# Kernel tuning notes

Hardware: AMD Instinct MI355X
Metric: run time of the kernel (lower is better)

Reference implementation:

```python
import jax, jax.numpy as jnp
import numpy as np

B, S, D_IN, D_OUT, H = 2, 2048, 1024, 1024, 16
DH = D_OUT // H

def setup_inputs() -> dict:
    key = jax.random.key(0)
    ks = jax.random.split(key, 6)
    sc = 0.02
    return {
        'x': jax.random.normal(ks[0], (B, S, D_IN), dtype=jnp.float32),
        'Wq': jax.random.normal(ks[1], (D_IN, D_OUT), dtype=jnp.float32) * sc,
        'Wk': jax.random.normal(ks[2], (D_IN, D_OUT), dtype=jnp.float32) * sc,
        'Wv': jax.random.normal(ks[3], (D_IN, D_OUT), dtype=jnp.float32) * sc,
        'Wo': jax.random.normal(ks[4], (D_OUT, D_OUT), dtype=jnp.float32) * sc,
        'bo': jax.random.normal(ks[5], (D_OUT,), dtype=jnp.float32) * sc,
    }

def reference(x, Wq, Wk, Wv, Wo, bo):
    b, s, _ = x.shape
    # projections, split heads: (b, h, s, dh)
    q = (x @ Wq).reshape(b, s, H, DH).transpose(0, 2, 1, 3)
    k = (x @ Wk).reshape(b, s, H, DH).transpose(0, 2, 1, 3)
    v = (x @ Wv).reshape(b, s, H, DH).transpose(0, 2, 1, 3)
    scores = jnp.einsum('bhqd,bhkd->bhqk', q, k)
    causal = jnp.triu(jnp.ones((s, s), dtype=bool), k=1)
    scores = jnp.where(causal, -jnp.inf, scores)
    attn = jax.nn.softmax(scores / jnp.sqrt(jnp.float32(DH)), axis=-1)
    ctx = jnp.einsum('bhqk,bhkd->bhqd', attn, v)
    ctx = ctx.transpose(0, 2, 1, 3).reshape(b, s, D_OUT)
    return ctx @ Wo + bo
```

## Files before the change

### kernel.cpp

```cpp
#include <hip/hip_runtime.h>
#include <hip/hip_bf16.h>
#include <cstdint>

typedef __attribute__((ext_vector_type(8))) __bf16 bf16x8;
typedef __attribute__((ext_vector_type(4))) float f32x4;
typedef __attribute__((ext_vector_type(8))) unsigned short u16x8;
typedef __attribute__((ext_vector_type(4))) unsigned short u16x4;
typedef __attribute__((ext_vector_type(4))) unsigned int u32x4;

#define NEG_INF (-__builtin_inff())

__device__ __forceinline__ unsigned short f2bf(float f) {
    unsigned int u = __builtin_bit_cast(unsigned int, f);
    u += 0x7FFFu + ((u >> 16) & 1u);
    return (unsigned short)(u >> 16);
}
__device__ __forceinline__ float bf2f(unsigned short u) {
    return __builtin_bit_cast(float, (unsigned int)u << 16);
}

__device__ __forceinline__ void gload16(const void* g, void* l) {
    __builtin_amdgcn_global_load_lds(
        (__attribute__((address_space(1))) void*)(uintptr_t)g,
        (__attribute__((address_space(3))) void*)(uint32_t)(uintptr_t)l, 16, 0, 0);
}

__global__ void cast_x_kernel(const float* __restrict__ x, unsigned short* __restrict__ xb) {
    size_t i = (size_t)blockIdx.x * 256 + threadIdx.x;
    const float4* p = (const float4*)x + i * 2;
    float4 a = p[0], c = p[1];
    u16x8 o;
    o[0] = f2bf(a.x); o[1] = f2bf(a.y); o[2] = f2bf(a.z); o[3] = f2bf(a.w);
    o[4] = f2bf(c.x); o[5] = f2bf(c.y); o[6] = f2bf(c.z); o[7] = f2bf(c.w);
    ((u16x8*)xb)[i] = o;
}

__global__ void castT_w_kernel(const float* __restrict__ W0, const float* __restrict__ W1,
                               const float* __restrict__ W2, const float* __restrict__ W3,
                               unsigned short* __restrict__ Wcat, unsigned short* __restrict__ Wot) {
    __shared__ float t[32][33];
    int z = blockIdx.z;
    const float* src = (z == 0) ? W0 : (z == 1) ? W1 : (z == 2) ? W2 : W3;
    unsigned short* dst = (z < 3) ? (Wcat + (size_t)z * 1024 * 1024) : Wot;
    int n0 = blockIdx.x * 32, k0 = blockIdx.y * 32;
    int tx = threadIdx.x & 31, ty = threadIdx.x >> 5;
    #pragma unroll
    for (int i = 0; i < 4; ++i) {
        int r = ty + i * 8;
        t[r][tx] = src[(size_t)(k0 + r) * 1024 + n0 + tx];
    }
    __syncthreads();
    #pragma unroll
    for (int i = 0; i < 4; ++i) {
        int r = ty + i * 8;
        dst[(size_t)(n0 + r) * 1024 + k0 + tx] = f2bf(t[tx][r]);
    }
}

__global__ __launch_bounds__(256, 2)
void gemm_qkv_kernel(const unsigned short* __restrict__ A, const unsigned short* __restrict__ Bt,
                     unsigned short* __restrict__ Qb, unsigned short* __restrict__ Kb,
                     unsigned short* __restrict__ Vtb) {
    __shared__ unsigned short As[128 * 64];
    __shared__ unsigned short Bs[128 * 64];
    const int tid = threadIdx.x;
    const int w = tid >> 6, l = tid & 63;
    const int lr = l & 15, lg = l >> 4;
    const int wr = w >> 1, wc = w & 1;
    const int id = blockIdx.y * 24 + blockIdx.x;
    const int swz = (id & 7) * 96 + (id >> 3);
    const int m0 = (swz / 24) * 128;
    const int n0 = (swz % 24) * 128;
    const int K = 1024;

    f32x4 acc[4][4] = {};

    for (int k0 = 0; k0 < 1024; k0 += 64) {
        #pragma unroll
        for (int p = 0; p < 4; ++p) {
            int seg = p * 4 + w;
            int row = seg * 8 + (l >> 3);
            int c16 = (l & 7) ^ (row & 7);
            gload16(A  + (size_t)(m0 + row) * K + k0 + c16 * 8, &As[seg * 512]);
            gload16(Bt + (size_t)(n0 + row) * K + k0 + c16 * 8, &Bs[seg * 512]);
        }
        __syncthreads();
        #pragma unroll
        for (int ks = 0; ks < 2; ++ks) {
            bf16x8 af[4], bfr[4];
            #pragma unroll
            for (int i = 0; i < 4; ++i) {
                int ra = wr * 64 + i * 16 + lr;
                af[i] = *(const bf16x8*)&As[ra * 64 + (((ks << 2) | lg) ^ (ra & 7)) * 8];
                int rb = wc * 64 + i * 16 + lr;
                bfr[i] = *(const bf16x8*)&Bs[rb * 64 + (((ks << 2) | lg) ^ (rb & 7)) * 8];
            }
            #pragma unroll
            for (int i = 0; i < 4; ++i)
                #pragma unroll
                for (int j = 0; j < 4; ++j)
                    acc[i][j] = __builtin_amdgcn_mfma_f32_16x16x32_bf16(af[i], bfr[j], acc[i][j], 0, 0, 0);
        }
        __syncthreads();
    }

    const int seg = n0 >> 10;
    const int n0l = n0 & 1023;
    if (seg < 2) {
        unsigned short* C = (seg == 0) ? Qb : Kb;
        const float sc = (seg == 0) ? 0.125f * 1.44269504f : 1.0f;
        #pragma unroll
        for (int i = 0; i < 4; ++i)
            #pragma unroll
            for (int j = 0; j < 4; ++j) {
                int n = n0l + wc * 64 + j * 16 + lr;
                #pragma unroll
                for (int r = 0; r < 4; ++r) {
                    int m = m0 + wr * 64 + i * 16 + lg * 4 + r;
                    C[(size_t)m * 1024 + n] = f2bf(acc[i][j][r] * sc);
                }
            }
    } else {
        #pragma unroll
        for (int i = 0; i < 4; ++i)
            #pragma unroll
            for (int j = 0; j < 4; ++j) {
                int n = n0l + wc * 64 + j * 16 + lr;
                int mb = m0 + wr * 64 + i * 16 + lg * 4;
                int bb = mb >> 11, s = mb & 2047;
                int s6 = s & 63;
                int kp = (((s6 >> 4) & 1) << 5) | (((s6 >> 2) & 3) << 3) | (((s6 >> 5) & 1) << 2);
                int sp = (s & ~63) | kp;
                u16x4 o;
                #pragma unroll
                for (int r = 0; r < 4; ++r) o[r] = f2bf(acc[i][j][r]);
                *(u16x4*)&Vtb[((size_t)(bb * 1024 + n)) * 2048 + sp] = o;
            }
    }
}

static __device__ const unsigned char QS_TAB[24] = {
    7,15,14,14,13,6,12,5,
    15,13,12,10,11,10,11,9,
    0,1,2,3,8,8,9,4};
static __device__ const unsigned char TY_TAB[24] = {
    0,2,1,2,2,0,2,0,
    1,1,1,1,1,2,2,2,
    0,0,0,0,1,2,1,0};

__global__ __launch_bounds__(256, 4)
void flash_attn_kernel(const unsigned short* __restrict__ Q, const unsigned short* __restrict__ Kg,
                       const unsigned short* __restrict__ Vt, unsigned short* __restrict__ ctx,
                       unsigned short* __restrict__ P_O, float* __restrict__ P_ml) {
    __shared__ unsigned short Ks[2][4096];
    __shared__ unsigned short Vs[2][4096];
    const int tid = threadIdx.x, w = tid >> 6, l = tid & 63;
    const int lr = l & 15, lg = l >> 4;

    const int level = blockIdx.x >> 5;
    const int bh = blockIdx.x & 31;
    const int qs = QS_TAB[level], ty = TY_TAB[level];
    const int Tf = 2 * qs + 2, mid = qs + 1;
    const int t0 = (ty == 2) ? mid : 0;
    const int t1 = (ty == 1) ? mid : Tf;
    const int b = bh >> 4, h = bh & 15;
    const int qw = qs * 128 + w * 32;

    const int srow8 = w * 8 + (l >> 3);
    const int scol  = (l & 7) ^ (srow8 & 7);
    const unsigned short* Kbase = Kg + (size_t)(b * 2048) * 1024 + h * 64;
    const unsigned short* Vbase = Vt + (size_t)(b * 1024 + h * 64) * 2048;

    const __bf16 one = (__bf16)1.0f;
    const bf16x8 ones = {one, one, one, one, one, one, one, one};

    bf16x8 qf[2][2];
    #pragma unroll
    for (int mi = 0; mi < 2; ++mi)
        #pragma unroll
        for (int ks = 0; ks < 2; ++ks)
            qf[mi][ks] = *(const bf16x8*)&Q[(size_t)(b * 2048 + qw + mi * 16 + lr) * 1024 + h * 64 + ks * 32 + lg * 8];

    float mrow[2] = {NEG_INF, NEG_INF};
    f32x4 lacc[2] = {};
    f32x4 oacc[2][4] = {};

    #pragma unroll
    for (int p = 0; p < 2; ++p)
        gload16(Kbase + (size_t)(t0 * 64 + p * 32 + srow8) * 1024 + scol * 8, &Ks[0][(p * 32 + w * 8) * 64]);

    for (int t = t0; t < t1; ++t) {
        const int cur = (t - t0) & 1;
        const int k0 = t * 64;
        #pragma unroll
        for (int p = 0; p < 2; ++p)
            gload16(Vbase + (size_t)(p * 32 + srow8) * 2048 + k0 + scol * 8, &Vs[cur][(p * 32 + w * 8) * 64]);
        const int ktn = (t + 1 < t1) ? t + 1 : t0;
        #pragma unroll
        for (int p = 0; p < 2; ++p)
            gload16(Kbase + (size_t)(ktn * 64 + p * 32 + srow8) * 1024 + scol * 8, &Ks[cur ^ 1][(p * 32 + w * 8) * 64]);

        asm volatile("s_waitcnt vmcnt(4)" ::: "memory");
        __builtin_amdgcn_s_barrier();

        f32x4 sf[2][4] = {};
        #pragma unroll
        for (int ks = 0; ks < 2; ++ks) {
            bf16x8 kf[4];
            #pragma unroll
            for (int ni = 0; ni < 4; ++ni) {
                int rk = ni * 16 + lr;
                kf[ni] = *(const bf16x8*)&Ks[cur][rk * 64 + (((ks << 2) | lg) ^ (rk & 7)) * 8];
            }
            #pragma unroll
            for (int ni = 0; ni < 4; ++ni)
                #pragma unroll
                for (int mi = 0; mi < 2; ++mi)
                    sf[mi][ni] = __builtin_amdgcn_mfma_f32_16x16x32_bf16(kf[ni], qf[mi][ks], sf[mi][ni], 0, 0, 0);
        }

        u32x4 pa0u[2], pa1u[2];
        #pragma unroll
        for (int mi = 0; mi < 2; ++mi) {
            if (t >= Tf - 2) {
                #pragma unroll
                for (int ni = 0; ni < 4; ++ni)
                    #pragma unroll
                    for (int r = 0; r < 4; ++r)
                        if (k0 + ni * 16 + lg * 4 + r > qw + mi * 16 + lr) sf[mi][ni][r] = NEG_INF;
            }
            float vmax = fmaxf(fmaxf(fmaxf(sf[mi][0][0], sf[mi][0][1]), fmaxf(sf[mi][0][2], sf[mi][0][3])),
                               fmaxf(fmaxf(sf[mi][1][0], sf[mi][1][1]), fmaxf(sf[mi][1][2], sf[mi][1][3])));
            vmax = fmaxf(vmax, fmaxf(fmaxf(fmaxf(sf[mi][2][0], sf[mi][2][1]), fmaxf(sf[mi][2][2], sf[mi][2][3])),
                                     fmaxf(fmaxf(sf[mi][3][0], sf[mi][3][1]), fmaxf(sf[mi][3][2], sf[mi][3][3]))));
            vmax = fmaxf(vmax, __shfl_xor(vmax, 16));
            vmax = fmaxf(vmax, __shfl_xor(vmax, 32));
            if (!__all(vmax <= mrow[mi] + 8.0f)) {
                float mn = fmaxf(mrow[mi], vmax);
                float av = __builtin_amdgcn_exp2f(mrow[mi] - mn);
                mrow[mi] = mn;
                float avr[4];
                #pragma unroll
                for (int r = 0; r < 4; ++r) avr[r] = __shfl(av, lg * 4 + r);
                #pragma unroll
                for (int ni = 0; ni < 4; ++ni)
                    #pragma unroll
                    for (int r = 0; r < 4; ++r)
                        oacc[mi][ni][r] *= avr[r];
                #pragma unroll
                for (int r = 0; r < 4; ++r) lacc[mi][r] *= avr[r];
            }
            #pragma unroll
            for (int ni = 0; ni < 4; ++ni)
                #pragma unroll
                for (int r = 0; r < 4; ++r)
                    sf[mi][ni][r] = __builtin_amdgcn_exp2f(sf[mi][ni][r] - mrow[mi]);

            asm("v_cvt_pk_bf16_f32 %0, %1, %2" : "=v"(pa0u[mi][0]) : "v"(sf[mi][0][0]), "v"(sf[mi][0][1]));
            asm("v_cvt_pk_bf16_f32 %0, %1, %2" : "=v"(pa0u[mi][1]) : "v"(sf[mi][0][2]), "v"(sf[mi][0][3]));
            asm("v_cvt_pk_bf16_f32 %0, %1, %2" : "=v"(pa0u[mi][2]) : "v"(sf[mi][2][0]), "v"(sf[mi][2][1]));
            asm("v_cvt_pk_bf16_f32 %0, %1, %2" : "=v"(pa0u[mi][3]) : "v"(sf[mi][2][2]), "v"(sf[mi][2][3]));
            asm("v_cvt_pk_bf16_f32 %0, %1, %2" : "=v"(pa1u[mi][0]) : "v"(sf[mi][1][0]), "v"(sf[mi][1][1]));
            asm("v_cvt_pk_bf16_f32 %0, %1, %2" : "=v"(pa1u[mi][1]) : "v"(sf[mi][1][2]), "v"(sf[mi][1][3]));
            asm("v_cvt_pk_bf16_f32 %0, %1, %2" : "=v"(pa1u[mi][2]) : "v"(sf[mi][3][0]), "v"(sf[mi][3][1]));
            asm("v_cvt_pk_bf16_f32 %0, %1, %2" : "=v"(pa1u[mi][3]) : "v"(sf[mi][3][2]), "v"(sf[mi][3][3]));

            lacc[mi] = __builtin_amdgcn_mfma_f32_16x16x32_bf16(
                __builtin_bit_cast(bf16x8, pa0u[mi]), ones, lacc[mi], 0, 0, 0);
            lacc[mi] = __builtin_amdgcn_mfma_f32_16x16x32_bf16(
                __builtin_bit_cast(bf16x8, pa1u[mi]), ones, lacc[mi], 0, 0, 0);
        }

        asm volatile("s_waitcnt vmcnt(2)" ::: "memory");
        __builtin_amdgcn_s_barrier();

        #pragma unroll
        for (int ks = 0; ks < 2; ++ks) {
            bf16x8 vb[4];
            #pragma unroll
            for (int ni = 0; ni < 4; ++ni) {
                int rv = ni * 16 + lr;
                vb[ni] = *(const bf16x8*)&Vs[cur][rv * 64 + (((ks << 2) | lg) ^ (rv & 7)) * 8];
            }
            #pragma unroll
            for (int mi = 0; mi < 2; ++mi) {
                bf16x8 pa = __builtin_bit_cast(bf16x8, ks ? pa1u[mi] : pa0u[mi]);
                #pragma unroll
                for (int ni = 0; ni < 4; ++ni)
                    oacc[mi][ni] = __builtin_amdgcn_mfma_f32_16x16x32_bf16(pa, vb[ni], oacc[mi][ni], 0, 0, 0);
            }
        }
    }

    if (ty == 0) {
        #pragma unroll
        for (int mi = 0; mi < 2; ++mi)
            #pragma unroll
            for (int r = 0; r < 4; ++r) {
                float inv = 1.0f / lacc[mi][r];
                int q = qw + mi * 16 + lg * 4 + r;
                size_t base = (size_t)(b * 2048 + q) * 1024 + h * 64 + lr;
                #pragma unroll
                for (int ni = 0; ni < 4; ++ni)
                    ctx[base + ni * 16] = f2bf(oacc[mi][ni][r] * inv);
            }
    } else {
        const int pidx = ((qs - 8) * 32 + bh) * 2 + (ty - 1);
        unsigned short* po = P_O + (size_t)pidx * 8192;
        #pragma unroll
        for (int mi = 0; mi < 2; ++mi)
            #pragma unroll
            for (int r = 0; r < 4; ++r) {
                int rowl = w * 32 + mi * 16 + lg * 4 + r;
                #pragma unroll
                for (int ni = 0; ni < 4; ++ni)
                    po[rowl * 64 + ni * 16 + lr] = f2bf(oacc[mi][ni][r]);
            }
        if (lg == 0) {
            #pragma unroll
            for (int mi = 0; mi < 2; ++mi)
                P_ml[pidx * 256 + (w * 32 + mi * 16 + lr) * 2] = mrow[mi];
        }
        if (lr == 0) {
            #pragma unroll
            for (int mi = 0; mi < 2; ++mi)
                #pragma unroll
                for (int r = 0; r < 4; ++r)
                    P_ml[pidx * 256 + (w * 32 + mi * 16 + lg * 4 + r) * 2 + 1] = lacc[mi][r];
        }
    }
}

__global__ __launch_bounds__(256)
void combine_kernel(const unsigned short* __restrict__ P_O, const float* __restrict__ P_ml,
                    unsigned short* __restrict__ ctx) {
    const int qs = 8 + (blockIdx.x >> 5);
    const int bh = blockIdx.x & 31;
    const int b = bh >> 4, h = bh & 15;
    const int p0 = ((qs - 8) * 32 + bh) * 2, p1 = p0 + 1;
    const int t = threadIdx.x;
    const int row = t >> 1, half = t & 1;
    const float m0 = P_ml[p0 * 256 + row * 2], l0 = P_ml[p0 * 256 + row * 2 + 1];
    const float m1 = P_ml[p1 * 256 + row * 2], l1 = P_ml[p1 * 256 + row * 2 + 1];
    const float m = fmaxf(m0, m1);
    float f0 = __builtin_amdgcn_exp2f(m0 - m);
    float f1 = __builtin_amdgcn_exp2f(m1 - m);
    const float inv = 1.0f / (l0 * f0 + l1 * f1);
    f0 *= inv; f1 *= inv;
    const u16x8* o0 = (const u16x8*)&P_O[(size_t)p0 * 8192 + row * 64 + half * 32];
    const u16x8* o1 = (const u16x8*)&P_O[(size_t)p1 * 8192 + row * 64 + half * 32];
    unsigned short* dst = ctx + (size_t)(b * 2048 + qs * 128 + row) * 1024 + h * 64 + half * 32;
    #pragma unroll
    for (int v = 0; v < 4; ++v) {
        u16x8 a = o0[v], c = o1[v], o;
        #pragma unroll
        for (int j = 0; j < 8; ++j)
            o[j] = f2bf(bf2f(a[j]) * f0 + bf2f(c[j]) * f1);
        ((u16x8*)dst)[v] = o;
    }
}

__global__ __launch_bounds__(256, 2)
void gemm_out_kernel(const unsigned short* __restrict__ A, const unsigned short* __restrict__ Bt,
                     float* __restrict__ C, const float* __restrict__ bias) {
    __shared__ unsigned short As[128 * 64];
    __shared__ unsigned short Bs[128 * 64];
    const int tid = threadIdx.x;
    const int w = tid >> 6, l = tid & 63;
    const int lr = l & 15, lg = l >> 4;
    const int wr = w >> 1, wc = w & 1;
    const int id = blockIdx.y * 8 + blockIdx.x;
    const int swz = (id & 7) * 32 + (id >> 3);
    const int m0 = (swz / 8) * 128;
    const int n0 = (swz % 8) * 128;
    const int K = 1024;

    f32x4 acc[4][4] = {};

    for (int k0 = 0; k0 < 1024; k0 += 64) {
        #pragma unroll
        for (int p = 0; p < 4; ++p) {
            int seg = p * 4 + w;
            int row = seg * 8 + (l >> 3);
            int c16 = (l & 7) ^ (row & 7);
            gload16(A  + (size_t)(m0 + row) * K + k0 + c16 * 8, &As[seg * 512]);
            gload16(Bt + (size_t)(n0 + row) * K + k0 + c16 * 8, &Bs[seg * 512]);
        }
        __syncthreads();
        #pragma unroll
        for (int ks = 0; ks < 2; ++ks) {
            bf16x8 af[4], bfr[4];
            #pragma unroll
            for (int i = 0; i < 4; ++i) {
                int ra = wr * 64 + i * 16 + lr;
                af[i] = *(const bf16x8*)&As[ra * 64 + (((ks << 2) | lg) ^ (ra & 7)) * 8];
                int rb = wc * 64 + i * 16 + lr;
                bfr[i] = *(const bf16x8*)&Bs[rb * 64 + (((ks << 2) | lg) ^ (rb & 7)) * 8];
            }
            #pragma unroll
            for (int i = 0; i < 4; ++i)
                #pragma unroll
                for (int j = 0; j < 4; ++j)
                    acc[i][j] = __builtin_amdgcn_mfma_f32_16x16x32_bf16(af[i], bfr[j], acc[i][j], 0, 0, 0);
        }
        __syncthreads();
    }

    #pragma unroll
    for (int i = 0; i < 4; ++i)
        #pragma unroll
        for (int j = 0; j < 4; ++j) {
            int n = n0 + wc * 64 + j * 16 + lr;
            float bv = bias[n];
            #pragma unroll
            for (int r = 0; r < 4; ++r) {
                int m = m0 + wr * 64 + i * 16 + lg * 4 + r;
                C[(size_t)m * 1024 + n] = acc[i][j][r] + bv;
            }
        }
}

extern "C" void kernel_launch(void* const* d_in, const int* in_sizes, int n_in,
                              void* d_out, int out_size, void* d_ws, size_t ws_size,
                              hipStream_t stream) {
    (void)in_sizes; (void)n_in; (void)out_size; (void)ws_size;
    const float* x  = (const float*)d_in[0];
    const float* Wq = (const float*)d_in[1];
    const float* Wk = (const float*)d_in[2];
    const float* Wv = (const float*)d_in[3];
    const float* Wo = (const float*)d_in[4];
    const float* bo = (const float*)d_in[5];
    float* out = (float*)d_out;

    char* ws = (char*)d_ws;
    const size_t MB = 1024 * 1024;
    unsigned short* xb   = (unsigned short*)(ws);
    unsigned short* Wcat = (unsigned short*)(ws + 8  * MB);
    unsigned short* Wot  = (unsigned short*)(ws + 14 * MB);
    unsigned short* Qb   = (unsigned short*)(ws + 16 * MB);
    unsigned short* Kb   = (unsigned short*)(ws + 24 * MB);
    unsigned short* Vtb  = (unsigned short*)(ws + 32 * MB);
    unsigned short* Cxb  = (unsigned short*)(ws + 40 * MB);

    unsigned short* P_O  = (unsigned short*)(ws);
    float*          P_ml = (float*)(ws + 8 * MB);

    cast_x_kernel<<<2048, 256, 0, stream>>>(x, xb);
    castT_w_kernel<<<dim3(32, 32, 4), 256, 0, stream>>>(Wq, Wk, Wv, Wo, Wcat, Wot);
    gemm_qkv_kernel<<<dim3(24, 32), 256, 0, stream>>>(xb, Wcat, Qb, Kb, Vtb);
    flash_attn_kernel<<<768, 256, 0, stream>>>(Qb, Kb, Vtb, Cxb, P_O, P_ml);
    combine_kernel<<<256, 256, 0, stream>>>(P_O, P_ml, Cxb);
    gemm_out_kernel<<<dim3(8, 32), 256, 0, stream>>>(Cxb, Wot, out, bo);
}
```

Measured before the change: 97.84 us.

## Split long causal query tiles into up to three KV chunks with three-way combine

Replaces the 2-way split-KV scheme (applied only to query tiles 8-15) with a finer one: tiles 5-10 split into two KV chunks and tiles 11-15 into three, giving 1024 attention blocks that are more evenly balanced. Chunk 0 writes unnormalized output straight into ctx and the other chunks go to a partial buffer, so the combine kernel reads ctx in place and merges two or three partials using the saved max and sum statistics. The aim is to shorten the tail of the causal workload and fill the GPU better. The cost is more partial traffic, a larger combine launch and extra bf16 rounding of the intermediate outputs.

```diff
diff --git a/kernel.cpp b/kernel.cpp
--- a/kernel.cpp
+++ b/kernel.cpp
@@ -139,14 +139,16 @@
     }
 }
 
-static __device__ const unsigned char QS_TAB[24] = {
-    7,15,14,14,13,6,12,5,
-    15,13,12,10,11,10,11,9,
-    0,1,2,3,8,8,9,4};
-static __device__ const unsigned char TY_TAB[24] = {
-    0,2,1,2,2,0,2,0,
-    1,1,1,1,1,2,2,2,
-    0,0,0,0,1,2,1,0};
+static __device__ const unsigned char QS_TAB[32] = {
+    15,15,14,14,14,15,13,13,
+    10,10,13, 9, 9,12,12, 8,
+     4,12,11,11,11, 7, 8, 7,
+     0, 1, 5, 5, 2, 6, 6, 3};
+static __device__ const unsigned char CI_TAB[32] = {
+     1, 2, 0, 1, 2, 0, 0, 1,
+     0, 1, 2, 0, 1, 1, 2, 0,
+     0, 0, 0, 1, 2, 0, 1, 1,
+     0, 0, 0, 1, 0, 0, 1, 0};
 
 __global__ __launch_bounds__(256, 4)
 void flash_attn_kernel(const unsigned short* __restrict__ Q, const unsigned short* __restrict__ Kg,
@@ -159,10 +161,11 @@
 
     const int level = blockIdx.x >> 5;
     const int bh = blockIdx.x & 31;
-    const int qs = QS_TAB[level], ty = TY_TAB[level];
-    const int Tf = 2 * qs + 2, mid = qs + 1;
-    const int t0 = (ty == 2) ? mid : 0;
-    const int t1 = (ty == 1) ? mid : Tf;
+    const int qs = QS_TAB[level], ci = CI_TAB[level];
+    const int c  = (qs >= 11) ? 3 : (qs >= 5 ? 2 : 1);
+    const int Tf = 2 * qs + 2;
+    const int t0 = (Tf * ci) / c;
+    const int t1 = (Tf * (ci + 1)) / c;
     const int b = bh >> 4, h = bh & 15;
     const int qw = qs * 128 + w * 32;
 
@@ -292,7 +295,7 @@
         }
     }
 
-    if (ty == 0) {
+    if (c == 1) {
         #pragma unroll
         for (int mi = 0; mi < 2; ++mi)
             #pragma unroll
@@ -305,28 +308,43 @@
                     ctx[base + ni * 16] = f2bf(oacc[mi][ni][r] * inv);
             }
     } else {
-        const int pidx = ((qs - 8) * 32 + bh) * 2 + (ty - 1);
-        unsigned short* po = P_O + (size_t)pidx * 8192;
-        #pragma unroll
-        for (int mi = 0; mi < 2; ++mi)
-            #pragma unroll
-            for (int r = 0; r < 4; ++r) {
-                int rowl = w * 32 + mi * 16 + lg * 4 + r;
-                #pragma unroll
-                for (int ni = 0; ni < 4; ++ni)
-                    po[rowl * 64 + ni * 16 + lr] = f2bf(oacc[mi][ni][r]);
-            }
+        if (ci == 0) {
+            #pragma unroll
+            for (int mi = 0; mi < 2; ++mi)
+                #pragma unroll
+                for (int r = 0; r < 4; ++r) {
+                    int q = qw + mi * 16 + lg * 4 + r;
+                    size_t base = (size_t)(b * 2048 + q) * 1024 + h * 64 + lr;
+                    #pragma unroll
+                    for (int ni = 0; ni < 4; ++ni)
+                        ctx[base + ni * 16] = f2bf(oacc[mi][ni][r]);
+                }
+        } else {
+            const int poslot = (qs <= 10) ? (qs - 5) : (6 + (qs - 11) * 2 + (ci - 1));
+            unsigned short* po = P_O + (size_t)(bh * 16 + poslot) * 8192;
+            #pragma unroll
+            for (int mi = 0; mi < 2; ++mi)
+                #pragma unroll
+                for (int r = 0; r < 4; ++r) {
+                    int rowl = w * 32 + mi * 16 + lg * 4 + r;
+                    #pragma unroll
+                    for (int ni = 0; ni < 4; ++ni)
+                        po[rowl * 64 + ni * 16 + lr] = f2bf(oacc[mi][ni][r]);
+                }
+        }
+        const int mlbase = (qs <= 10) ? (qs - 5) * 2 : (12 + (qs - 11) * 3);
+        float* mlp = P_ml + (size_t)(bh * 27 + mlbase + ci) * 256;
         if (lg == 0) {
             #pragma unroll
             for (int mi = 0; mi < 2; ++mi)
-                P_ml[pidx * 256 + (w * 32 + mi * 16 + lr) * 2] = mrow[mi];
+                mlp[(w * 32 + mi * 16 + lr) * 2] = mrow[mi];
         }
         if (lr == 0) {
             #pragma unroll
             for (int mi = 0; mi < 2; ++mi)
                 #pragma unroll
                 for (int r = 0; r < 4; ++r)
-                    P_ml[pidx * 256 + (w * 32 + mi * 16 + lg * 4 + r) * 2 + 1] = lacc[mi][r];
+                    mlp[(w * 32 + mi * 16 + lg * 4 + r) * 2 + 1] = lacc[mi][r];
         }
     }
 }
@@ -334,28 +352,48 @@
 __global__ __launch_bounds__(256)
 void combine_kernel(const unsigned short* __restrict__ P_O, const float* __restrict__ P_ml,
                     unsigned short* __restrict__ ctx) {
-    const int qs = 8 + (blockIdx.x >> 5);
+    const int qs = 5 + (blockIdx.x >> 5);
     const int bh = blockIdx.x & 31;
     const int b = bh >> 4, h = bh & 15;
-    const int p0 = ((qs - 8) * 32 + bh) * 2, p1 = p0 + 1;
+    const int c = (qs >= 11) ? 3 : 2;
     const int t = threadIdx.x;
     const int row = t >> 1, half = t & 1;
-    const float m0 = P_ml[p0 * 256 + row * 2], l0 = P_ml[p0 * 256 + row * 2 + 1];
-    const float m1 = P_ml[p1 * 256 + row * 2], l1 = P_ml[p1 * 256 + row * 2 + 1];
-    const float m = fmaxf(m0, m1);
-    float f0 = __builtin_amdgcn_exp2f(m0 - m);
-    float f1 = __builtin_amdgcn_exp2f(m1 - m);
-    const float inv = 1.0f / (l0 * f0 + l1 * f1);
-    f0 *= inv; f1 *= inv;
-    const u16x8* o0 = (const u16x8*)&P_O[(size_t)p0 * 8192 + row * 64 + half * 32];
-    const u16x8* o1 = (const u16x8*)&P_O[(size_t)p1 * 8192 + row * 64 + half * 32];
+
+    const int mlbase = (qs <= 10) ? (qs - 5) * 2 : (12 + (qs - 11) * 3);
+    float mv[3], lv[3];
+    #pragma unroll
+    for (int ci = 0; ci < 3; ++ci) {
+        if (ci < c) {
+            const float* mlp = P_ml + (size_t)(bh * 27 + mlbase + ci) * 256 + row * 2;
+            mv[ci] = mlp[0]; lv[ci] = mlp[1];
+        } else { mv[ci] = NEG_INF; lv[ci] = 0.0f; }
+    }
+    float m = fmaxf(fmaxf(mv[0], mv[1]), mv[2]);
+    float f0 = __builtin_amdgcn_exp2f(mv[0] - m);
+    float f1 = __builtin_amdgcn_exp2f(mv[1] - m);
+    float f2 = (c == 3) ? __builtin_amdgcn_exp2f(mv[2] - m) : 0.0f;
+    const float inv = 1.0f / (lv[0] * f0 + lv[1] * f1 + lv[2] * f2);
+    f0 *= inv; f1 *= inv; f2 *= inv;
+
     unsigned short* dst = ctx + (size_t)(b * 2048 + qs * 128 + row) * 1024 + h * 64 + half * 32;
+    const int pobase = (qs <= 10) ? (qs - 5) : (6 + (qs - 11) * 2);
+    const u16x8* s1 = (const u16x8*)&P_O[(size_t)(bh * 16 + pobase) * 8192 + row * 64 + half * 32];
+    const u16x8* s2 = (const u16x8*)&P_O[(size_t)(bh * 16 + pobase + 1) * 8192 + row * 64 + half * 32];
     #pragma unroll
     for (int v = 0; v < 4; ++v) {
-        u16x8 a = o0[v], c = o1[v], o;
-        #pragma unroll
-        for (int j = 0; j < 8; ++j)
-            o[j] = f2bf(bf2f(a[j]) * f0 + bf2f(c[j]) * f1);
+        u16x8 a = ((const u16x8*)dst)[v];
+        u16x8 o1 = s1[v];
+        u16x8 o;
+        if (c == 3) {
+            u16x8 o2 = s2[v];
+            #pragma unroll
+            for (int j = 0; j < 8; ++j)
+                o[j] = f2bf(bf2f(a[j]) * f0 + bf2f(o1[j]) * f1 + bf2f(o2[j]) * f2);
+        } else {
+            #pragma unroll
+            for (int j = 0; j < 8; ++j)
+                o[j] = f2bf(bf2f(a[j]) * f0 + bf2f(o1[j]) * f1);
+        }
         ((u16x8*)dst)[v] = o;
     }
 }
@@ -448,7 +486,7 @@
     cast_x_kernel<<<2048, 256, 0, stream>>>(x, xb);
     castT_w_kernel<<<dim3(32, 32, 4), 256, 0, stream>>>(Wq, Wk, Wv, Wo, Wcat, Wot);
     gemm_qkv_kernel<<<dim3(24, 32), 256, 0, stream>>>(xb, Wcat, Qb, Kb, Vtb);
-    flash_attn_kernel<<<768, 256, 0, stream>>>(Qb, Kb, Vtb, Cxb, P_O, P_ml);
-    combine_kernel<<<256, 256, 0, stream>>>(P_O, P_ml, Cxb);
+    flash_attn_kernel<<<1024, 256, 0, stream>>>(Qb, Kb, Vtb, Cxb, P_O, P_ml);
+    combine_kernel<<<352, 256, 0, stream>>>(P_O, P_ml, Cxb);
     gemm_out_kernel<<<dim3(8, 32), 256, 0, stream>>>(Cxb, Wot, out, bo);
 }
```

Result: slower. 102.0 us (+4.3%).
